# Kernel optimization log

Measured on AMD Instinct MI355X. Metric: run time of the kernel, lower is better.

The kernel has to match this reference:

```python
import jax, jax.numpy as jnp
import numpy as np

N = 4096  # num_neurons
THRESHOLD = 0.0  # torch forward default


def setup_inputs() -> dict:
    key = jax.random.key(0)
    k1, k2 = jax.random.split(key)
    W = jax.random.normal(k1, (N, N), dtype=jnp.float32)
    # Hopfield weights have zero self-connections (fill_diagonal_(0))
    W = W * (1.0 - jnp.eye(N, dtype=jnp.float32))
    x = jax.random.normal(k2, (N,), dtype=jnp.float32)
    return {"input_pattern": x, "weights": W, "max_iterations": 4}


def reference(input_pattern, weights, max_iterations):
    n = weights.shape[0]

    # One asynchronous neuron update: uses the CURRENT (partially updated) state.
    def neuron_step(state, i):
        activation = jnp.dot(weights[i], state)  # row-i dot current state
        state = state.at[i].set(jnp.sign(activation - THRESHOLD))
        return state, None

    # One full sweep over all neurons, in order 0..n-1 (asynchronous updates).
    def sweep(state, _):
        state, _ = jax.lax.scan(neuron_step, state, jnp.arange(n))
        return state, None

    # Fixed number of sweeps. A converged state is a fixed point of `sweep`,
    # so this matches the torch early-break loop's final output exactly.
    state, _ = jax.lax.scan(sweep, input_pattern, None, length=max_iterations)
    return state
```

## Files before the change

### kernel.cpp

```cpp
#include <hip/hip_runtime.h>

#define NN 4096
#define BB 128
#define GG 32
#define MAXT 8
#define MAXE (MAXT * GG)
#define MASK63 0x7FFFFFFFFFFFFFFFull
#define MASK62 0x3FFFFFFFFFFFFFFFull
#define TOPBIT 0x8000000000000000ull

__global__ __launch_bounds__(256)
void hop_init(const float* __restrict__ x, const float* __restrict__ W,
              unsigned long long* __restrict__ slots, float* __restrict__ partial_buf)
{
    const int tid = threadIdx.x, bid = blockIdx.x;
    const int lane = tid & 63, w = tid >> 6;
    const int lam = lane & 31, half = lane >> 5;

    if (bid == 0) {
        for (int i = tid; i < MAXE * 8; i += 256) slots[i] = 0ull;
    }

    const int tm = bid >> 3, tc = bid & 7;
    const int rbase = tm * BB, cbase = tc * 512;

    float4 xv[4];
#pragma unroll
    for (int u = 0; u < 4; ++u)
        xv[u] = *(const float4*)(x + cbase + 4 * lam + 128 * u);

#pragma unroll 2
    for (int it = 0; it < 16; ++it) {
        const int r = w * 32 + it * 2 + half;
        const float* wrow = W + (size_t)(rbase + r) * NN + cbase;
        float p = 0.f;
#pragma unroll
        for (int u = 0; u < 4; ++u) {
            float4 wv = *(const float4*)(wrow + 4 * lam + 128 * u);
            p = fmaf(wv.x, xv[u].x, p); p = fmaf(wv.y, xv[u].y, p);
            p = fmaf(wv.z, xv[u].z, p); p = fmaf(wv.w, xv[u].w, p);
        }
#pragma unroll
        for (int s = 16; s; s >>= 1) p += __shfl_xor(p, s);
        if (lam == 0) partial_buf[(size_t)bid * BB + r] = p;
    }
}

__global__ __launch_bounds__(256)
void hop_main(const float* __restrict__ x, const float* __restrict__ W,
              const int* __restrict__ maxit, float* __restrict__ out,
              unsigned long long* __restrict__ slots,
              const float* __restrict__ partial_buf)
{
    __shared__ float wdT[BB][BB + 1];
    __shared__ float pbuf[2][NN];
    __shared__ float a_lds[BB];
    __shared__ float delta_lds[BB];
    __shared__ unsigned long long mbox[2][2];
    __shared__ unsigned long long pm[2][GG][2];
    __shared__ int   status_lds;

    const int tid = threadIdx.x;
    const int m = blockIdx.x;
    const int lane = tid & 63, w = tid >> 6;
    const int lam = lane & 31, half = lane >> 5;
    const int bm = m * BB;

    int T = *maxit; if (T > MAXT) T = MAXT; if (T < 0) T = 0;
    const long long tstart = clock64();

    for (int l = tid; l < BB * BB; l += 256) {
        const int i = l >> 7, j = l & 127;
        wdT[j][i] = W[(size_t)(bm + i) * NN + bm + j];
    }
    for (int i = tid; i < NN; i += 256) pbuf[0][i] = x[i];
    if (tid < BB) {
        float s = 0.f;
#pragma unroll
        for (int c = 0; c < 8; ++c) s += partial_buf[(size_t)(m * 8 + c) * BB + tid];
        a_lds[tid] = s;
    }
    float sold0 = 0.f, sold1 = 0.f;
    if (w == 0) { sold0 = x[bm + lane]; sold1 = x[bm + 64 + lane]; }
    __syncthreads();

    for (int e = 0; e < T * GG; ++e) {
        const int k = e & (GG - 1);
        const int s = e >> 5;
        if (k != m) {
            float4 wpre[16];
#pragma unroll
            for (int it = 0; it < 16; ++it) {
                const int r = w * 32 + it * 2 + half;
                wpre[it] = *(const float4*)(W + (size_t)(bm + r) * NN + k * BB + 4 * lam);
            }
            if (w == 0) {
                const unsigned long long* sl = slots + (size_t)e * 8;
                const int dist = (m - k + GG) & (GG - 1);
                unsigned long long q0, q1, q2;
                long long iters = 0;
                for (;;) {
                    q0 = __hip_atomic_load(&sl[0], __ATOMIC_RELAXED, __HIP_MEMORY_SCOPE_AGENT);
                    q1 = __hip_atomic_load(&sl[1], __ATOMIC_RELAXED, __HIP_MEMORY_SCOPE_AGENT);
                    q2 = __hip_atomic_load(&sl[2], __ATOMIC_RELAXED, __HIP_MEMORY_SCOPE_AGENT);
                    if ((q0 & q1 & q2) >> 63) break;
                    if (dist == 1)      __builtin_amdgcn_s_sleep(1);
                    else if (dist <= 4) __builtin_amdgcn_s_sleep(4);
                    else                __builtin_amdgcn_s_sleep(32);
                    if (((++iters) & 63) == 0 && (clock64() - tstart) > 500000000LL) break;
                }
                const unsigned long long mm0 = (q0 & MASK63) | (q1 << 63);
                const unsigned long long mm1 = ((q1 >> 1) & MASK62) | (q2 << 62);
                if (lane == 0) {
                    mbox[e & 1][0] = mm0;
                    mbox[e & 1][1] = mm1;
                    pm[s & 1][k][0] = mm0;
                    pm[s & 1][k][1] = mm1;
                }
            }
            __syncthreads();
            const unsigned long long m0 = mbox[e & 1][0];
            const unsigned long long m1 = mbox[e & 1][1];
            const bool any = (s == 0) ||
                             (m0 != pm[(s - 1) & 1][k][0]) ||
                             (m1 != pm[(s - 1) & 1][k][1]);

            const int jc = 4 * lam;
            const float4 pv = *(const float4*)&pbuf[s & 1][k * BB + jc];
            float4 d4;
            {
                const float s0 = ((jc + 0 < 64 ? (m0 >> (jc + 0)) : (m1 >> (jc - 64))) & 1) ? 1.f : -1.f;
                const float s1 = ((jc + 1 < 64 ? (m0 >> (jc + 1)) : (m1 >> (jc - 63))) & 1) ? 1.f : -1.f;
                const float s2 = ((jc + 2 < 64 ? (m0 >> (jc + 2)) : (m1 >> (jc - 62))) & 1) ? 1.f : -1.f;
                const float s3 = ((jc + 3 < 64 ? (m0 >> (jc + 3)) : (m1 >> (jc - 61))) & 1) ? 1.f : -1.f;
                d4.x = s0 - pv.x; d4.y = s1 - pv.y; d4.z = s2 - pv.z; d4.w = s3 - pv.w;
            }
            if (tid < BB) {
                const int b = tid < 64 ? (int)((m0 >> tid) & 1) : (int)((m1 >> (tid - 64)) & 1);
                pbuf[(s + 1) & 1][k * BB + tid] = b ? 1.f : -1.f;
            }
            if (any) {
#pragma unroll
                for (int it = 0; it < 16; ++it) {
                    const int r = w * 32 + it * 2 + half;
                    const float4 wv = wpre[it];
                    float p = fmaf(wv.x, d4.x, fmaf(wv.y, d4.y, fmaf(wv.z, d4.z, wv.w * d4.w)));
#pragma unroll
                    for (int sh = 16; sh; sh >>= 1) p += __shfl_xor(p, sh);
                    if (lam == 0) a_lds[r] += p;
                }
            }
        } else {
            __syncthreads();
            if (w == 0) {
                float c0 = a_lds[lane], c1 = a_lds[lane + 64];
                const float dp0 = 1.f - sold0, dm0 = -1.f - sold0;
                const float dp1 = 1.f - sold1, dm1 = -1.f - sold1;
                const float cand0 = c0 > 0.f ? dp0 : dm0;
                const float cand1 = c1 > 0.f ? dp1 : dm1;
                const unsigned long long bz = __ballot((cand0 != 0.f) || (cand1 != 0.f));
                float vdf0 = 0.f, vdf1 = 0.f;
                const int zero_all = (bz == 0ULL);
                if (!zero_all) {
                    float vsn0 = sold0, vsn1 = sold1;
                    float pw0[6], pw1[6];
#pragma unroll
                    for (int u = 0; u < 6; ++u) { pw0[u] = wdT[u][lane]; pw1[u] = wdT[u][lane + 64]; }
#pragma unroll
                    for (int j = 0; j < 64; ++j) {
                        const float dq = c0 > 0.f ? dp0 : dm0;
                        const float sq = c0 > 0.f ? 1.f : -1.f;
                        const float bc = __int_as_float(
                            __builtin_amdgcn_readlane(__float_as_int(dq), j));
                        const bool me = (lane == j);
                        vdf0 = me ? dq : vdf0;
                        vsn0 = me ? sq : vsn0;
                        const float w0 = pw0[j % 6], w1 = pw1[j % 6];
                        pw0[j % 6] = wdT[j + 6][lane];
                        pw1[j % 6] = wdT[j + 6][lane + 64];
                        c0 = fmaf(w0, bc, c0);
                        c1 = fmaf(w1, bc, c1);
                    }
                    const float cnd1 = c1 > 0.f ? dp1 : dm1;
                    const unsigned long long bz1 = __ballot(cnd1 != 0.f);
                    if (bz1 != 0ULL) {
#pragma unroll
                        for (int j = 64; j < 128; ++j) {
                            const float dq = c1 > 0.f ? dp1 : dm1;
                            const float sq = c1 > 0.f ? 1.f : -1.f;
                            const float bc = __int_as_float(
                                __builtin_amdgcn_readlane(__float_as_int(dq), j & 63));
                            const bool me = (lane == (j & 63));
                            vdf1 = me ? dq : vdf1;
                            vsn1 = me ? sq : vsn1;
                            const float w1 = pw1[j % 6];
                            if (j + 6 < BB) pw1[j % 6] = wdT[j + 6][lane + 64];
                            c1 = fmaf(w1, bc, c1);
                        }
                    }
                    sold0 = vsn0;
                    sold1 = vsn1;
                }
                {
                    const unsigned long long pm0 = __ballot(sold0 > 0.f);
                    const unsigned long long pm1 = __ballot(sold1 > 0.f);
                    unsigned long long* sl = slots + (size_t)e * 8;
                    if (lane == 0) {
                        __hip_atomic_store(&sl[0], TOPBIT | (pm0 & MASK63),
                                           __ATOMIC_RELAXED, __HIP_MEMORY_SCOPE_AGENT);
                        __hip_atomic_store(&sl[1], TOPBIT | (pm0 >> 63) | ((pm1 & MASK62) << 1),
                                           __ATOMIC_RELAXED, __HIP_MEMORY_SCOPE_AGENT);
                        __hip_atomic_store(&sl[2], TOPBIT | (pm1 >> 62),
                                           __ATOMIC_RELAXED, __HIP_MEMORY_SCOPE_AGENT);
                    }
                }
                if (lane == 0) status_lds = zero_all;
                if (!zero_all) {
                    delta_lds[lane] = vdf0;
                    delta_lds[lane + 64] = vdf1;
                }
            }
            __syncthreads();
            if (!status_lds) {
                float dv[4];
#pragma unroll
                for (int u = 0; u < 4; ++u) dv[u] = delta_lds[lam + 32 * u];
#pragma unroll 2
                for (int it = 0; it < 16; ++it) {
                    const int r = w * 32 + it * 2 + half;
                    float p = 0.f;
#pragma unroll
                    for (int u = 0; u < 4; ++u) p = fmaf(wdT[lam + 32 * u][r], dv[u], p);
#pragma unroll
                    for (int sh = 16; sh; sh >>= 1) p += __shfl_xor(p, sh);
                    if (lam == 0) a_lds[r] += p;
                }
            }
        }
    }

    if (w == 0) {
        out[bm + lane] = sold0;
        out[bm + 64 + lane] = sold1;
    }
}

extern "C" void kernel_launch(void* const* d_in, const int* in_sizes, int n_in,
                              void* d_out, int out_size, void* d_ws, size_t ws_size,
                              hipStream_t stream) {
    const float* x = (const float*)d_in[0];
    const float* W = (const float*)d_in[1];
    const int* maxit = (const int*)d_in[2];
    float* out = (float*)d_out;

    char* ws = (char*)d_ws;
    unsigned long long* slots = (unsigned long long*)ws;
    float* partial_buf = (float*)(ws + (size_t)MAXE * 8 * 8);
    if (ws_size < (size_t)(MAXE * 64 + 256 * BB * 4)) return;

    hipLaunchKernelGGL(hop_init, dim3(256), dim3(256), 0, stream,
                       x, W, slots, partial_buf);

    void* args[6];
    args[0] = (void*)&x; args[1] = (void*)&W; args[2] = (void*)&maxit;
    args[3] = (void*)&out; args[4] = (void*)&slots; args[5] = (void*)&partial_buf;
    (void)hipLaunchCooperativeKernel(hop_main, dim3(GG), dim3(256), args, 0u, stream);
}
```

Baseline: 1.060 ms.

## Add dedicated polling wave and skip W prefetch after quiet sweeps

Adds a fifth wavefront that alone handles slot polling, the diagonal sequential update and the state bookkeeping, while the other four waves do the off-diagonal accumulation. It also tracks whether anything changed during the previous full sweep and, if nothing did, skips the per-step prefetch of the W tile. This targets polling latency on the compute waves and redundant global loads once the state has converged. In exchange it adds cross-wave coordination through shared memory and a quiet flag computed one sweep behind.

```diff
diff --git a/kernel.cpp b/kernel.cpp
--- a/kernel.cpp
+++ b/kernel.cpp
@@ -5,6 +5,7 @@
 #define GG 32
 #define MAXT 8
 #define MAXE (MAXT * GG)
+#define NTH 320
 #define MASK63 0x7FFFFFFFFFFFFFFFull
 #define MASK62 0x3FFFFFFFFFFFFFFFull
 #define TOPBIT 0x8000000000000000ull
@@ -46,7 +47,7 @@
     }
 }
 
-__global__ __launch_bounds__(256)
+__global__ __launch_bounds__(NTH)
 void hop_main(const float* __restrict__ x, const float* __restrict__ W,
               const int* __restrict__ maxit, float* __restrict__ out,
               unsigned long long* __restrict__ slots,
@@ -59,6 +60,7 @@
     __shared__ unsigned long long mbox[2][2];
     __shared__ unsigned long long pm[2][GG][2];
     __shared__ int   status_lds;
+    __shared__ int   quiet_lds;
 
     const int tid = threadIdx.x;
     const int m = blockIdx.x;
@@ -69,19 +71,21 @@
     int T = *maxit; if (T > MAXT) T = MAXT; if (T < 0) T = 0;
     const long long tstart = clock64();
 
-    for (int l = tid; l < BB * BB; l += 256) {
+    for (int l = tid; l < BB * BB; l += NTH) {
         const int i = l >> 7, j = l & 127;
         wdT[j][i] = W[(size_t)(bm + i) * NN + bm + j];
     }
-    for (int i = tid; i < NN; i += 256) pbuf[0][i] = x[i];
+    for (int i = tid; i < NN; i += NTH) pbuf[0][i] = x[i];
     if (tid < BB) {
         float s = 0.f;
 #pragma unroll
         for (int c = 0; c < 8; ++c) s += partial_buf[(size_t)(m * 8 + c) * BB + tid];
         a_lds[tid] = s;
     }
+    if (tid == 0) quiet_lds = 0;
     float sold0 = 0.f, sold1 = 0.f;
-    if (w == 0) { sold0 = x[bm + lane]; sold1 = x[bm + 64 + lane]; }
+    if (w == 4) { sold0 = x[bm + lane]; sold1 = x[bm + 64 + lane]; }
+    int swchg = 1;
     __syncthreads();
 
     for (int e = 0; e < T * GG; ++e) {
@@ -89,12 +93,16 @@
         const int s = e >> 5;
         if (k != m) {
             float4 wpre[16];
-#pragma unroll
-            for (int it = 0; it < 16; ++it) {
-                const int r = w * 32 + it * 2 + half;
-                wpre[it] = *(const float4*)(W + (size_t)(bm + r) * NN + k * BB + 4 * lam);
-            }
-            if (w == 0) {
+            const int quiet = quiet_lds;
+            if (w < 4) {
+                if (!quiet) {
+#pragma unroll
+                    for (int it = 0; it < 16; ++it) {
+                        const int r = w * 32 + it * 2 + half;
+                        wpre[it] = *(const float4*)(W + (size_t)(bm + r) * NN + k * BB + 4 * lam);
+                    }
+                }
+            } else {
                 const unsigned long long* sl = slots + (size_t)e * 8;
                 const int dist = (m - k + GG) & (GG - 1);
                 unsigned long long q0, q1, q2;
@@ -111,12 +119,18 @@
                 }
                 const unsigned long long mm0 = (q0 & MASK63) | (q1 << 63);
                 const unsigned long long mm1 = ((q1 >> 1) & MASK62) | (q2 << 62);
+                const int chg = (s == 0) ||
+                                (mm0 != pm[(s - 1) & 1][k][0]) ||
+                                (mm1 != pm[(s - 1) & 1][k][1]);
+                swchg |= chg;
                 if (lane == 0) {
                     mbox[e & 1][0] = mm0;
                     mbox[e & 1][1] = mm1;
                     pm[s & 1][k][0] = mm0;
                     pm[s & 1][k][1] = mm1;
-                }
+                    if (k == GG - 1) quiet_lds = !swchg;
+                }
+                if (k == GG - 1) swchg = 0;
             }
             __syncthreads();
             const unsigned long long m0 = mbox[e & 1][0];
@@ -125,21 +139,19 @@
                              (m0 != pm[(s - 1) & 1][k][0]) ||
                              (m1 != pm[(s - 1) & 1][k][1]);
 
-            const int jc = 4 * lam;
-            const float4 pv = *(const float4*)&pbuf[s & 1][k * BB + jc];
-            float4 d4;
-            {
+            if (tid < BB) {
+                const int b = tid < 64 ? (int)((m0 >> tid) & 1) : (int)((m1 >> (tid - 64)) & 1);
+                pbuf[(s + 1) & 1][k * BB + tid] = b ? 1.f : -1.f;
+            }
+            if (w < 4 && any) {
+                const int jc = 4 * lam;
+                const float4 pv = *(const float4*)&pbuf[s & 1][k * BB + jc];
+                float4 d4;
                 const float s0 = ((jc + 0 < 64 ? (m0 >> (jc + 0)) : (m1 >> (jc - 64))) & 1) ? 1.f : -1.f;
                 const float s1 = ((jc + 1 < 64 ? (m0 >> (jc + 1)) : (m1 >> (jc - 63))) & 1) ? 1.f : -1.f;
                 const float s2 = ((jc + 2 < 64 ? (m0 >> (jc + 2)) : (m1 >> (jc - 62))) & 1) ? 1.f : -1.f;
                 const float s3 = ((jc + 3 < 64 ? (m0 >> (jc + 3)) : (m1 >> (jc - 61))) & 1) ? 1.f : -1.f;
                 d4.x = s0 - pv.x; d4.y = s1 - pv.y; d4.z = s2 - pv.z; d4.w = s3 - pv.w;
-            }
-            if (tid < BB) {
-                const int b = tid < 64 ? (int)((m0 >> tid) & 1) : (int)((m1 >> (tid - 64)) & 1);
-                pbuf[(s + 1) & 1][k * BB + tid] = b ? 1.f : -1.f;
-            }
-            if (any) {
 #pragma unroll
                 for (int it = 0; it < 16; ++it) {
                     const int r = w * 32 + it * 2 + half;
@@ -152,7 +164,7 @@
             }
         } else {
             __syncthreads();
-            if (w == 0) {
+            if (w == 4) {
                 float c0 = a_lds[lane], c1 = a_lds[lane + 64];
                 const float dp0 = 1.f - sold0, dm0 = -1.f - sold0;
                 const float dp1 = 1.f - sold1, dm1 = -1.f - sold1;
@@ -214,14 +226,19 @@
                                            __ATOMIC_RELAXED, __HIP_MEMORY_SCOPE_AGENT);
                     }
                 }
-                if (lane == 0) status_lds = zero_all;
+                swchg |= !zero_all;
+                if (lane == 0) {
+                    status_lds = zero_all;
+                    if (k == GG - 1) quiet_lds = !swchg;
+                }
+                if (k == GG - 1) swchg = 0;
                 if (!zero_all) {
                     delta_lds[lane] = vdf0;
                     delta_lds[lane + 64] = vdf1;
                 }
             }
             __syncthreads();
-            if (!status_lds) {
+            if (w < 4 && !status_lds) {
                 float dv[4];
 #pragma unroll
                 for (int u = 0; u < 4; ++u) dv[u] = delta_lds[lam + 32 * u];
@@ -239,7 +256,7 @@
         }
     }
 
-    if (w == 0) {
+    if (w == 4) {
         out[bm + lane] = sold0;
         out[bm + 64 + lane] = sold1;
     }
@@ -255,7 +272,7 @@
 
     char* ws = (char*)d_ws;
     unsigned long long* slots = (unsigned long long*)ws;
-    float* partial_buf = (float*)(ws + (size_t)MAXE * 8 * 8);
+    float* partial_buf = (float*)(ws + (size_t)MAXE * 64);
     if (ws_size < (size_t)(MAXE * 64 + 256 * BB * 4)) return;
 
     hipLaunchKernelGGL(hop_init, dim3(256), dim3(256), 0, stream,
@@ -264,5 +281,5 @@
     void* args[6];
     args[0] = (void*)&x; args[1] = (void*)&W; args[2] = (void*)&maxit;
     args[3] = (void*)&out; args[4] = (void*)&slots; args[5] = (void*)&partial_buf;
-    (void)hipLaunchCooperativeKernel(hop_main, dim3(GG), dim3(256), args, 0u, stream);
+    (void)hipLaunchCooperativeKernel(hop_main, dim3(GG), dim3(NTH), args, 0u, stream);
 }
```

Result: slower. 1.117 ms (+5.4%).

## Split hop_main into producer wave and four consumer waves with LDS flag sync

Applied to the files above, without the earlier changes.

Restructures the persistent kernel into warp specialization. Wave 0 polls the global slots, builds the delta vector and runs the diagonal-block sequential update. Four extra waves apply the off-diagonal rank updates to the local activations and prefetch the next W tile. Block-wide __syncthreads is replaced by workgroup-scope sequence counters (delta_seq, applied_seq), and the slot poll checks one acquire load instead of three. The diagonal block now uses only a register-based update, with no second LDS pass. The aim is to overlap polling and the serial critical path with the matrix-vector work and to take barriers off the chain between blocks. The cost is more threads, spin-waiting inside the workgroup and subtle memory-ordering risk.

```diff
diff --git a/kernel.cpp b/kernel.cpp
--- a/kernel.cpp
+++ b/kernel.cpp
@@ -5,13 +5,17 @@
 #define GG 32
 #define MAXT 8
 #define MAXE (MAXT * GG)
+#define NTH 320
 #define MASK63 0x7FFFFFFFFFFFFFFFull
 #define MASK62 0x3FFFFFFFFFFFFFFFull
 #define TOPBIT 0x8000000000000000ull
 
+typedef unsigned long long ull;
+typedef unsigned long long ull2 __attribute__((ext_vector_type(2)));
+
 __global__ __launch_bounds__(256)
 void hop_init(const float* __restrict__ x, const float* __restrict__ W,
-              unsigned long long* __restrict__ slots, float* __restrict__ partial_buf)
+              ull* __restrict__ slots, float* __restrict__ partial_buf)
 {
     const int tid = threadIdx.x, bid = blockIdx.x;
     const int lane = tid & 63, w = tid >> 6;
@@ -46,120 +50,103 @@
     }
 }
 
-__global__ __launch_bounds__(256)
+__global__ __launch_bounds__(NTH)
 void hop_main(const float* __restrict__ x, const float* __restrict__ W,
               const int* __restrict__ maxit, float* __restrict__ out,
-              unsigned long long* __restrict__ slots,
-              const float* __restrict__ partial_buf)
+              ull* __restrict__ slots, const float* __restrict__ partial_buf)
 {
     __shared__ float wdT[BB][BB + 1];
-    __shared__ float pbuf[2][NN];
+    __shared__ float x_lds[NN];
     __shared__ float a_lds[BB];
-    __shared__ float delta_lds[BB];
-    __shared__ unsigned long long mbox[2][2];
-    __shared__ unsigned long long pm[2][GG][2];
-    __shared__ int   status_lds;
+    __shared__ float d_lds[BB];
+    __shared__ ull   pm[2][GG][2];
+    __shared__ int   delta_seq;
+    __shared__ int   delta_any;
+    __shared__ int   applied_seq[4];
 
     const int tid = threadIdx.x;
     const int m = blockIdx.x;
-    const int lane = tid & 63, w = tid >> 6;
+    const int lane = tid & 63, wv = tid >> 6;
     const int lam = lane & 31, half = lane >> 5;
     const int bm = m * BB;
 
     int T = *maxit; if (T > MAXT) T = MAXT; if (T < 0) T = 0;
+    const int TT = T * GG;
     const long long tstart = clock64();
 
-    for (int l = tid; l < BB * BB; l += 256) {
+    for (int l = tid; l < BB * BB; l += NTH) {
         const int i = l >> 7, j = l & 127;
         wdT[j][i] = W[(size_t)(bm + i) * NN + bm + j];
     }
-    for (int i = tid; i < NN; i += 256) pbuf[0][i] = x[i];
+    for (int i = tid; i < NN; i += NTH) x_lds[i] = x[i];
     if (tid < BB) {
         float s = 0.f;
 #pragma unroll
         for (int c = 0; c < 8; ++c) s += partial_buf[(size_t)(m * 8 + c) * BB + tid];
         a_lds[tid] = s;
     }
+    if (tid == 0) { delta_seq = -1; delta_any = 0; }
+    if (tid < 4) applied_seq[tid] = -1;
     float sold0 = 0.f, sold1 = 0.f;
-    if (w == 0) { sold0 = x[bm + lane]; sold1 = x[bm + 64 + lane]; }
+    if (wv == 0) { sold0 = x[bm + lane]; sold1 = x[bm + 64 + lane]; }
     __syncthreads();
 
-    for (int e = 0; e < T * GG; ++e) {
-        const int k = e & (GG - 1);
-        const int s = e >> 5;
-        if (k != m) {
-            float4 wpre[16];
-#pragma unroll
-            for (int it = 0; it < 16; ++it) {
-                const int r = w * 32 + it * 2 + half;
-                wpre[it] = *(const float4*)(W + (size_t)(bm + r) * NN + k * BB + 4 * lam);
-            }
-            if (w == 0) {
-                const unsigned long long* sl = slots + (size_t)e * 8;
+    if (wv == 0) {
+        for (int t = 0; t < TT; ++t) {
+            const int k = t & (GG - 1);
+            const int s = t >> 5;
+            for (int w = 0; w < 4; ++w) {
+                long long it2 = 0;
+                while (__hip_atomic_load(&applied_seq[w], __ATOMIC_ACQUIRE,
+                                         __HIP_MEMORY_SCOPE_WORKGROUP) < t - 1) {
+                    if (((++it2) & 255) == 0 && (clock64() - tstart) > 500000000LL) break;
+                }
+            }
+            if (k != m) {
+                const ull* sl = slots + (size_t)t * 8;
                 const int dist = (m - k + GG) & (GG - 1);
-                unsigned long long q0, q1, q2;
+                ull q2;
                 long long iters = 0;
                 for (;;) {
-                    q0 = __hip_atomic_load(&sl[0], __ATOMIC_RELAXED, __HIP_MEMORY_SCOPE_AGENT);
-                    q1 = __hip_atomic_load(&sl[1], __ATOMIC_RELAXED, __HIP_MEMORY_SCOPE_AGENT);
-                    q2 = __hip_atomic_load(&sl[2], __ATOMIC_RELAXED, __HIP_MEMORY_SCOPE_AGENT);
-                    if ((q0 & q1 & q2) >> 63) break;
+                    q2 = __hip_atomic_load(&sl[2], __ATOMIC_ACQUIRE,
+                                           __HIP_MEMORY_SCOPE_AGENT);
+                    if (q2 >> 63) break;
                     if (dist == 1)      __builtin_amdgcn_s_sleep(1);
                     else if (dist <= 4) __builtin_amdgcn_s_sleep(4);
                     else                __builtin_amdgcn_s_sleep(32);
                     if (((++iters) & 63) == 0 && (clock64() - tstart) > 500000000LL) break;
                 }
-                const unsigned long long mm0 = (q0 & MASK63) | (q1 << 63);
-                const unsigned long long mm1 = ((q1 >> 1) & MASK62) | (q2 << 62);
+                const ull2 q01 = *(const ull2*)sl;
+                const ull q0 = q01.x, q1 = q01.y;
+                const ull mm0 = (q0 & MASK63) | (q1 << 63);
+                const ull mm1 = ((q1 >> 1) & MASK62) | (q2 << 62);
+                const ull p0 = pm[(s - 1) & 1][k][0];
+                const ull p1 = pm[(s - 1) & 1][k][1];
+                const int any = (s == 0) || (mm0 != p0) || (mm1 != p1);
+                {
+                    const float c0 = ((mm0 >> lane) & 1) ? 1.f : -1.f;
+                    const float pr0 = (s == 0) ? x_lds[k * BB + lane]
+                                               : (((p0 >> lane) & 1) ? 1.f : -1.f);
+                    d_lds[lane] = c0 - pr0;
+                    const float c1 = ((mm1 >> lane) & 1) ? 1.f : -1.f;
+                    const float pr1 = (s == 0) ? x_lds[k * BB + 64 + lane]
+                                               : (((p1 >> lane) & 1) ? 1.f : -1.f);
+                    d_lds[64 + lane] = c1 - pr1;
+                }
                 if (lane == 0) {
-                    mbox[e & 1][0] = mm0;
-                    mbox[e & 1][1] = mm1;
                     pm[s & 1][k][0] = mm0;
                     pm[s & 1][k][1] = mm1;
-                }
-            }
-            __syncthreads();
-            const unsigned long long m0 = mbox[e & 1][0];
-            const unsigned long long m1 = mbox[e & 1][1];
-            const bool any = (s == 0) ||
-                             (m0 != pm[(s - 1) & 1][k][0]) ||
-                             (m1 != pm[(s - 1) & 1][k][1]);
-
-            const int jc = 4 * lam;
-            const float4 pv = *(const float4*)&pbuf[s & 1][k * BB + jc];
-            float4 d4;
-            {
-                const float s0 = ((jc + 0 < 64 ? (m0 >> (jc + 0)) : (m1 >> (jc - 64))) & 1) ? 1.f : -1.f;
-                const float s1 = ((jc + 1 < 64 ? (m0 >> (jc + 1)) : (m1 >> (jc - 63))) & 1) ? 1.f : -1.f;
-                const float s2 = ((jc + 2 < 64 ? (m0 >> (jc + 2)) : (m1 >> (jc - 62))) & 1) ? 1.f : -1.f;
-                const float s3 = ((jc + 3 < 64 ? (m0 >> (jc + 3)) : (m1 >> (jc - 61))) & 1) ? 1.f : -1.f;
-                d4.x = s0 - pv.x; d4.y = s1 - pv.y; d4.z = s2 - pv.z; d4.w = s3 - pv.w;
-            }
-            if (tid < BB) {
-                const int b = tid < 64 ? (int)((m0 >> tid) & 1) : (int)((m1 >> (tid - 64)) & 1);
-                pbuf[(s + 1) & 1][k * BB + tid] = b ? 1.f : -1.f;
-            }
-            if (any) {
-#pragma unroll
-                for (int it = 0; it < 16; ++it) {
-                    const int r = w * 32 + it * 2 + half;
-                    const float4 wv = wpre[it];
-                    float p = fmaf(wv.x, d4.x, fmaf(wv.y, d4.y, fmaf(wv.z, d4.z, wv.w * d4.w)));
-#pragma unroll
-                    for (int sh = 16; sh; sh >>= 1) p += __shfl_xor(p, sh);
-                    if (lam == 0) a_lds[r] += p;
-                }
-            }
-        } else {
-            __syncthreads();
-            if (w == 0) {
+                    delta_any = any;
+                    __hip_atomic_store(&delta_seq, t, __ATOMIC_RELEASE,
+                                       __HIP_MEMORY_SCOPE_WORKGROUP);
+                }
+            } else {
                 float c0 = a_lds[lane], c1 = a_lds[lane + 64];
                 const float dp0 = 1.f - sold0, dm0 = -1.f - sold0;
                 const float dp1 = 1.f - sold1, dm1 = -1.f - sold1;
                 const float cand0 = c0 > 0.f ? dp0 : dm0;
                 const float cand1 = c1 > 0.f ? dp1 : dm1;
-                const unsigned long long bz = __ballot((cand0 != 0.f) || (cand1 != 0.f));
-                float vdf0 = 0.f, vdf1 = 0.f;
+                const ull bz = __ballot((cand0 != 0.f) || (cand1 != 0.f));
                 const int zero_all = (bz == 0ULL);
                 if (!zero_all) {
                     float vsn0 = sold0, vsn1 = sold1;
@@ -173,7 +160,6 @@
                         const float bc = __int_as_float(
                             __builtin_amdgcn_readlane(__float_as_int(dq), j));
                         const bool me = (lane == j);
-                        vdf0 = me ? dq : vdf0;
                         vsn0 = me ? sq : vsn0;
                         const float w0 = pw0[j % 6], w1 = pw1[j % 6];
                         pw0[j % 6] = wdT[j + 6][lane];
@@ -182,7 +168,7 @@
                         c1 = fmaf(w1, bc, c1);
                     }
                     const float cnd1 = c1 > 0.f ? dp1 : dm1;
-                    const unsigned long long bz1 = __ballot(cnd1 != 0.f);
+                    const ull bz1 = __ballot(cnd1 != 0.f);
                     if (bz1 != 0ULL) {
 #pragma unroll
                         for (int j = 64; j < 128; ++j) {
@@ -191,57 +177,82 @@
                             const float bc = __int_as_float(
                                 __builtin_amdgcn_readlane(__float_as_int(dq), j & 63));
                             const bool me = (lane == (j & 63));
-                            vdf1 = me ? dq : vdf1;
                             vsn1 = me ? sq : vsn1;
-                            const float w1 = pw1[j % 6];
-                            if (j + 6 < BB) pw1[j % 6] = wdT[j + 6][lane + 64];
+                            const float w0 = pw0[j % 6], w1 = pw1[j % 6];
+                            if (j + 6 < BB) {
+                                pw0[j % 6] = wdT[j + 6][lane];
+                                pw1[j % 6] = wdT[j + 6][lane + 64];
+                            }
+                            c0 = fmaf(w0, bc, c0);
                             c1 = fmaf(w1, bc, c1);
                         }
                     }
-                    sold0 = vsn0;
-                    sold1 = vsn1;
+                    sold0 = vsn0; sold1 = vsn1;
+                    a_lds[lane] = c0;
+                    a_lds[lane + 64] = c1;
                 }
                 {
-                    const unsigned long long pm0 = __ballot(sold0 > 0.f);
-                    const unsigned long long pm1 = __ballot(sold1 > 0.f);
-                    unsigned long long* sl = slots + (size_t)e * 8;
+                    const ull b0 = __ballot(sold0 > 0.f);
+                    const ull b1 = __ballot(sold1 > 0.f);
+                    ull* sl = slots + (size_t)t * 8;
                     if (lane == 0) {
-                        __hip_atomic_store(&sl[0], TOPBIT | (pm0 & MASK63),
+                        __hip_atomic_store(&sl[0], TOPBIT | (b0 & MASK63),
                                            __ATOMIC_RELAXED, __HIP_MEMORY_SCOPE_AGENT);
-                        __hip_atomic_store(&sl[1], TOPBIT | (pm0 >> 63) | ((pm1 & MASK62) << 1),
+                        __hip_atomic_store(&sl[1], TOPBIT | (b0 >> 63) | ((b1 & MASK62) << 1),
                                            __ATOMIC_RELAXED, __HIP_MEMORY_SCOPE_AGENT);
-                        __hip_atomic_store(&sl[2], TOPBIT | (pm1 >> 62),
-                                           __ATOMIC_RELAXED, __HIP_MEMORY_SCOPE_AGENT);
+                        __hip_atomic_store(&sl[2], TOPBIT | (b1 >> 62),
+                                           __ATOMIC_RELEASE, __HIP_MEMORY_SCOPE_AGENT);
+                        pm[s & 1][k][0] = b0;
+                        pm[s & 1][k][1] = b1;
+                        delta_any = 0;
+                        __hip_atomic_store(&delta_seq, t, __ATOMIC_RELEASE,
+                                           __HIP_MEMORY_SCOPE_WORKGROUP);
                     }
                 }
-                if (lane == 0) status_lds = zero_all;
-                if (!zero_all) {
-                    delta_lds[lane] = vdf0;
-                    delta_lds[lane + 64] = vdf1;
-                }
-            }
-            __syncthreads();
-            if (!status_lds) {
-                float dv[4];
-#pragma unroll
-                for (int u = 0; u < 4; ++u) dv[u] = delta_lds[lam + 32 * u];
-#pragma unroll 2
+            }
+        }
+        out[bm + lane] = sold0;
+        out[bm + 64 + lane] = sold1;
+    } else {
+        const int w = wv - 1;
+        float4 wpre[16];
+#pragma unroll
+        for (int it = 0; it < 16; ++it) {
+            const int r = w * 32 + it * 2 + half;
+            wpre[it] = *(const float4*)(W + (size_t)(bm + r) * NN + 0 * BB + 4 * lam);
+        }
+        for (int t = 0; t < TT; ++t) {
+            long long iters = 0;
+            while (__hip_atomic_load(&delta_seq, __ATOMIC_ACQUIRE,
+                                     __HIP_MEMORY_SCOPE_WORKGROUP) < t) {
+                __builtin_amdgcn_s_sleep(1);
+                if (((++iters) & 255) == 0 && (clock64() - tstart) > 500000000LL) break;
+            }
+            if (delta_any) {
+                const float4 d4 = *(const float4*)&d_lds[4 * lam];
+#pragma unroll
                 for (int it = 0; it < 16; ++it) {
                     const int r = w * 32 + it * 2 + half;
-                    float p = 0.f;
-#pragma unroll
-                    for (int u = 0; u < 4; ++u) p = fmaf(wdT[lam + 32 * u][r], dv[u], p);
+                    const float4 wvv = wpre[it];
+                    float p = fmaf(wvv.x, d4.x, fmaf(wvv.y, d4.y,
+                              fmaf(wvv.z, d4.z, wvv.w * d4.w)));
 #pragma unroll
                     for (int sh = 16; sh; sh >>= 1) p += __shfl_xor(p, sh);
                     if (lam == 0) a_lds[r] += p;
                 }
             }
-        }
-    }
-
-    if (w == 0) {
-        out[bm + lane] = sold0;
-        out[bm + 64 + lane] = sold1;
+            if (lane == 0)
+                __hip_atomic_store(&applied_seq[w], t, __ATOMIC_RELEASE,
+                                   __HIP_MEMORY_SCOPE_WORKGROUP);
+            if (t + 1 < TT) {
+                const int kn = (t + 1) & (GG - 1);
+#pragma unroll
+                for (int it = 0; it < 16; ++it) {
+                    const int r = w * 32 + it * 2 + half;
+                    wpre[it] = *(const float4*)(W + (size_t)(bm + r) * NN + kn * BB + 4 * lam);
+                }
+            }
+        }
     }
 }
 
@@ -254,8 +265,8 @@
     float* out = (float*)d_out;
 
     char* ws = (char*)d_ws;
-    unsigned long long* slots = (unsigned long long*)ws;
-    float* partial_buf = (float*)(ws + (size_t)MAXE * 8 * 8);
+    ull* slots = (ull*)ws;
+    float* partial_buf = (float*)(ws + (size_t)MAXE * 64);
     if (ws_size < (size_t)(MAXE * 64 + 256 * BB * 4)) return;
 
     hipLaunchKernelGGL(hop_init, dim3(256), dim3(256), 0, stream,
@@ -264,5 +275,5 @@
     void* args[6];
     args[0] = (void*)&x; args[1] = (void*)&W; args[2] = (void*)&maxit;
     args[3] = (void*)&out; args[4] = (void*)&slots; args[5] = (void*)&partial_buf;
-    (void)hipLaunchCooperativeKernel(hop_main, dim3(GG), dim3(256), args, 0u, stream);
+    (void)hipLaunchCooperativeKernel(hop_main, dim3(GG), dim3(NTH), args, 0u, stream);
 }
```

New measurement: 1.165 ms. 1.1x slower.
